# Optimization experiments

Measured on AMD Instinct MI355X. Metric: run time of the kernel, lower is better.

Reference implementation:

```python
import jax, jax.numpy as jnp
import numpy as np

N_NODE = 100000
H = 128          # hidden_size
N_INTEREST = 4
B = 4096         # batch
T = 50           # session length


def setup_inputs() -> dict:
    key = jax.random.key(0)
    ks = jax.random.split(key, 8)
    stdv = 1.0 / np.sqrt(H)
    u = lambda k, s: jax.random.uniform(k, s, jnp.float32, -stdv, stdv)
    return {
        "inputs": jax.random.randint(ks[0], (B, T), 0, N_NODE),
        "embedding": u(ks[1], (N_NODE, H)),            # nn.Embedding weight
        "w_interest": u(ks[2], (N_INTEREST, H)),       # Linear(H -> n_interest, bias=False)
        "w_ih": u(ks[3], (N_INTEREST, 3 * H, H)),      # per-interest GNN params
        "w_hh": u(ks[4], (N_INTEREST, 3 * H, H)),
        "b_ih": u(ks[5], (N_INTEREST, 3 * H)),
        "b_hh": u(ks[6], (N_INTEREST, 3 * H)),
        "h0": jax.random.normal(ks[7], (N_INTEREST, B, H), jnp.float32),  # torch.randn init state
    }


def _gru_interest(w_ih, w_hh, b_ih, b_hh, h0, g_t, x_t):
    """Custom gated recurrence for one interest. x_t: [T,B,H], g_t: [T,B]."""
    def step(h, inp):
        x, gv = inp
        gi = x @ w_ih.T + b_ih          # [B, 3H]
        gh = h @ w_hh.T + b_hh          # [B, 3H]
        i_r, i_i, i_n = jnp.split(gi, 3, axis=1)
        h_r, h_i, h_n = jnp.split(gh, 3, axis=1)
        resetgate = jax.nn.sigmoid(i_r + h_r)
        inputgate = jax.nn.sigmoid(i_i + h_i)
        newgate = jnp.tanh(i_n + resetgate * h_n)
        g = gv[:, None]                  # [B, 1]
        concentrgate = jnp.where(g > 0.01, 1.0, 0.0) * g * inputgate
        hy = (1.0 - concentrgate) * h + concentrgate * newgate
        return hy, None
    h_last, _ = jax.lax.scan(step, h0, (x_t, g_t))
    return h_last                        # [B, H]


def reference(inputs, embedding, w_interest, w_ih, w_hh, b_ih, b_hh, h0):
    hidden = embedding[inputs]                                   # [B, T, H]
    # item_weight_for_interest: softmax over interests with temperature 0.1
    g = jax.nn.softmax((hidden @ w_interest.T) / 0.1, axis=2)    # [B, T, I]
    x_t = jnp.transpose(hidden, (1, 0, 2))                       # [T, B, H]
    g_t = jnp.transpose(g, (2, 1, 0))                            # [I, T, B]
    out = jax.vmap(_gru_interest, in_axes=(0, 0, 0, 0, 0, 0, None))(
        w_ih, w_hh, b_ih, b_hh, h0, g_t, x_t)                    # [I, B, H]
    return jnp.transpose(out, (1, 0, 2))                         # [B, I, H]
```

## Files before the change

### kernel.cpp

```cpp
#include <hip/hip_runtime.h>
#include <hip/hip_bf16.h>

#define NB 4096
#define NT 50
#define NH 128
#define NINT 4
#define ROWS 64

typedef float f32x4 __attribute__((ext_vector_type(4)));
typedef __bf16 bf16x8 __attribute__((ext_vector_type(8)));
typedef short short8 __attribute__((ext_vector_type(8)));
typedef short short4s __attribute__((ext_vector_type(4)));

#define L2E 1.4426950408889634f

__device__ __forceinline__ float frcp(float x) { return __builtin_amdgcn_rcpf(x); }

__device__ __forceinline__ float exp2neg(float x) {
  float r;
  asm("v_exp_f32 %0, -%1" : "=v"(r) : "v"(x));
  return r;
}

__device__ __forceinline__ unsigned short bfbits(float f) {
  __bf16 b = (__bf16)f;
  return __builtin_bit_cast(unsigned short, b);
}

__global__ __launch_bounds__(512, 2)
void gru_fused(const int* __restrict__ inputs, const float* __restrict__ emb,
               const float* __restrict__ w_int, const float* __restrict__ w_ih,
               const float* __restrict__ w_hh, const float* __restrict__ b_ih,
               const float* __restrict__ b_hh, const float* __restrict__ h0,
               float* __restrict__ out) {
  __shared__ unsigned short xs[2][ROWS * NH];
  __shared__ unsigned short hs[2][ROWS * NH];
  __shared__ float gbuf[2][ROWS];
  __shared__ float wintl[NINT][NH + 16];
  __shared__ int idxs[NT * ROWS];

  const int tid = threadIdx.x;
  const int bx = blockIdx.x;
  const int I = bx >> 6;
  const int R0 = (bx & 63) * ROWS;
  const int w = tid >> 6;
  const int lane = tid & 63;
  const int l15 = lane & 15;
  const int l4 = lane >> 4;
  const int oc0 = w * 16 + l4 * 4;

  const int sr = tid >> 3;
  const int sp = tid & 7;

  for (int e = tid; e < NT * ROWS; e += 512) {
    int t = e >> 6, r = e & (ROWS - 1);
    idxs[e] = inputs[(size_t)(R0 + r) * NT + t];
  }
  {
    int i = tid >> 7, f = tid & 127;
    wintl[i][f + ((f >> 5) << 2)] = w_int[tid];
  }
  __syncthreads();

  auto gate_from = [&](int buf, float4 a, float4 b, float4 c, float4 e) {
    const int wbase = sp * 16 + (sp >> 1) * 4;
    float d[NINT];
    #pragma unroll
    for (int i = 0; i < NINT; ++i) {
      const float4* wq = (const float4*)&wintl[i][wbase];
      float4 w0 = wq[0], w1 = wq[1], w2 = wq[2], w3 = wq[3];
      d[i] = a.x * w0.x + a.y * w0.y + a.z * w0.z + a.w * w0.w +
             b.x * w1.x + b.y * w1.y + b.z * w1.z + b.w * w1.w +
             c.x * w2.x + c.y * w2.y + c.z * w2.z + c.w * w2.w +
             e.x * w3.x + e.y * w3.y + e.z * w3.z + e.w * w3.w;
    }
    #pragma unroll
    for (int off = 1; off < 8; off <<= 1) {
      #pragma unroll
      for (int i = 0; i < NINT; ++i) d[i] += __shfl_xor(d[i], off, 64);
    }
    if (sp == 0) {
      float sa = d[0] * 10.f, sb = d[1] * 10.f, sc = d[2] * 10.f, sd = d[3] * 10.f;
      float mx = fmaxf(fmaxf(sa, sb), fmaxf(sc, sd));
      float ea = __expf(sa - mx), eb = __expf(sb - mx), ec = __expf(sc - mx),
            ed = __expf(sd - mx);
      float sel = (I == 0) ? ea : (I == 1) ? eb : (I == 2) ? ec : ed;
      float gv = sel * frcp(ea + eb + ec + ed);
      gbuf[buf][sr] = (gv > 0.01f) ? gv : 0.0f;
    }
  };

  bf16x8 wih[3][4], whh[3][4];
  f32x4 bR, bI, bNI, bNH;
  {
    const float gs[3] = {L2E, L2E, 2.0f * L2E};
    #pragma unroll
    for (int g = 0; g < 3; ++g) {
      int oc = g * NH + w * 16 + l15;
      #pragma unroll
      for (int kk = 0; kk < 4; ++kk) {
        int k0 = kk * 32 + l4 * 8;
        const float* pi = w_ih + ((size_t)(I * 384 + oc) * NH + k0);
        const float* ph = w_hh + ((size_t)(I * 384 + oc) * NH + k0);
        bf16x8 si, sh;
        #pragma unroll
        for (int e = 0; e < 8; ++e) {
          si[e] = (__bf16)(pi[e] * gs[g]);
          sh[e] = (__bf16)(ph[e] * gs[g]);
        }
        wih[g][kk] = si;
        whh[g][kk] = sh;
      }
    }
    #pragma unroll
    for (int j = 0; j < 4; ++j) {
      bR[j] = (b_ih[I * 384 + oc0 + j] + b_hh[I * 384 + oc0 + j]) * L2E;
      bI[j] = (b_ih[I * 384 + NH + oc0 + j] + b_hh[I * 384 + NH + oc0 + j]) * L2E;
      bNI[j] = b_ih[I * 384 + 2 * NH + oc0 + j] * (2.0f * L2E);
      bNH[j] = b_hh[I * 384 + 2 * NH + oc0 + j] * (2.0f * L2E);
    }
  }

  float hm[4][4];
  #pragma unroll
  for (int m = 0; m < 4; ++m) {
    int row = m * 16 + l15;
    short4s p;
    #pragma unroll
    for (int j = 0; j < 4; ++j) {
      float v = h0[((size_t)I * NB + R0 + row) * NH + oc0 + j];
      hm[m][j] = v;
      p[j] = (short)bfbits(v);
    }
    *(short4s*)&hs[0][(row * NH + oc0) ^ ((row & 7) << 3)] = p;
  }

  {
    const float4* src = (const float4*)(emb + (size_t)idxs[sr] * NH + sp * 16);
    float4 v0 = src[0], v1 = src[1], v2 = src[2], v3 = src[3];
    short8 s0, s1;
    s0[0] = bfbits(v0.x); s0[1] = bfbits(v0.y); s0[2] = bfbits(v0.z); s0[3] = bfbits(v0.w);
    s0[4] = bfbits(v1.x); s0[5] = bfbits(v1.y); s0[6] = bfbits(v1.z); s0[7] = bfbits(v1.w);
    s1[0] = bfbits(v2.x); s1[1] = bfbits(v2.y); s1[2] = bfbits(v2.z); s1[3] = bfbits(v2.w);
    s1[4] = bfbits(v3.x); s1[5] = bfbits(v3.y); s1[6] = bfbits(v3.z); s1[7] = bfbits(v3.w);
    int base = sr * NH + sp * 16;
    int sw = (sr & 7) << 3;
    *(short8*)&xs[0][base ^ sw] = s0;
    *(short8*)&xs[0][(base + 8) ^ sw] = s1;
    gate_from(0, v0, v1, v2, v3);
  }
  __syncthreads();

  for (int t = 0; t < NT; ++t) {
    const int cur = t & 1, nxt = cur ^ 1;
    const bool pf = (t + 1 < NT);

    float4 v0, v1, v2, v3;
    if (pf) {
      const float4* src =
          (const float4*)(emb + (size_t)idxs[(t + 1) * ROWS + sr] * NH + sp * 16);
      v0 = src[0]; v1 = src[1]; v2 = src[2]; v3 = src[3];
    }

    const unsigned short* hsc = hs[cur];
    const unsigned short* xsc = xs[cur];
    unsigned short* hsn = hs[nxt];

    #pragma unroll
    for (int m = 0; m < 4; ++m) {
      f32x4 aR = bR, aI = bI, aNI = bNI, aNH = bNH;

      int brow = m * 16 + l15;
      int blin = brow * NH + l4 * 8;
      int sw2 = (brow & 7) << 3;
      __builtin_amdgcn_s_setprio(1);
      #pragma unroll
      for (int kk = 0; kk < 4; ++kk) {
        int e = (blin + kk * 32) ^ sw2;
        bf16x8 bh = __builtin_bit_cast(bf16x8, *(const short8*)&hsc[e]);
        bf16x8 bx = __builtin_bit_cast(bf16x8, *(const short8*)&xsc[e]);
        aR = __builtin_amdgcn_mfma_f32_16x16x32_bf16(wih[0][kk], bx, aR, 0, 0, 0);
        aR = __builtin_amdgcn_mfma_f32_16x16x32_bf16(whh[0][kk], bh, aR, 0, 0, 0);
        aI = __builtin_amdgcn_mfma_f32_16x16x32_bf16(wih[1][kk], bx, aI, 0, 0, 0);
        aI = __builtin_amdgcn_mfma_f32_16x16x32_bf16(whh[1][kk], bh, aI, 0, 0, 0);
        aNI = __builtin_amdgcn_mfma_f32_16x16x32_bf16(wih[2][kk], bx, aNI, 0, 0, 0);
        aNH = __builtin_amdgcn_mfma_f32_16x16x32_bf16(whh[2][kk], bh, aNH, 0, 0, 0);
      }
      __builtin_amdgcn_s_setprio(0);

      const float gv = gbuf[cur][brow];
      short4s p;
      #pragma unroll
      for (int j = 0; j < 4; ++j) {
        float rg = frcp(1.0f + exp2neg(aR[j]));
        float ig = frcp(1.0f + exp2neg(aI[j]));
        float an = fmaf(rg, aNH[j], aNI[j]);
        float ng = fmaf(2.0f, frcp(1.0f + exp2neg(an)), -1.0f);
        float c = gv * ig;
        float hy = fmaf(c, ng - hm[m][j], hm[m][j]);
        hm[m][j] = hy;
        p[j] = (short)bfbits(hy);
      }
      *(short4s*)&hsn[(brow * NH + oc0) ^ sw2] = p;
    }

    if (pf) {
      short8 s0, s1;
      s0[0] = bfbits(v0.x); s0[1] = bfbits(v0.y); s0[2] = bfbits(v0.z); s0[3] = bfbits(v0.w);
      s0[4] = bfbits(v1.x); s0[5] = bfbits(v1.y); s0[6] = bfbits(v1.z); s0[7] = bfbits(v1.w);
      s1[0] = bfbits(v2.x); s1[1] = bfbits(v2.y); s1[2] = bfbits(v2.z); s1[3] = bfbits(v2.w);
      s1[4] = bfbits(v3.x); s1[5] = bfbits(v3.y); s1[6] = bfbits(v3.z); s1[7] = bfbits(v3.w);
      int base = sr * NH + sp * 16;
      int sw = (sr & 7) << 3;
      *(short8*)&xs[nxt][base ^ sw] = s0;
      *(short8*)&xs[nxt][(base + 8) ^ sw] = s1;
      gate_from(nxt, v0, v1, v2, v3);
    }
    __syncthreads();
  }

  #pragma unroll
  for (int m = 0; m < 4; ++m) {
    int row = m * 16 + l15;
    f32x4 o;
    #pragma unroll
    for (int j = 0; j < 4; ++j) o[j] = hm[m][j];
    *(f32x4*)&out[(size_t)(R0 + row) * (NINT * NH) + I * NH + oc0] = o;
  }
}

extern "C" void kernel_launch(void* const* d_in, const int* in_sizes, int n_in,
                              void* d_out, int out_size, void* d_ws, size_t ws_size,
                              hipStream_t stream) {
  const int* inputs = (const int*)d_in[0];
  const float* emb = (const float*)d_in[1];
  const float* w_int = (const float*)d_in[2];
  const float* w_ih = (const float*)d_in[3];
  const float* w_hh = (const float*)d_in[4];
  const float* b_ih = (const float*)d_in[5];
  const float* b_hh = (const float*)d_in[6];
  const float* h0 = (const float*)d_in[7];
  float* out = (float*)d_out;

  dim3 grid(NINT * (NB / ROWS));
  dim3 block(512);
  gru_fused<<<grid, block, 0, stream>>>(inputs, emb, w_int, w_ih, w_hh, b_ih,
                                        b_hh, h0, out);
}
```

Measured before the change: 192.6 us.

## Compute interest softmax gate with MFMA inside the recurrence loop

Replaces the per-step scalar dot-product, shuffle reduction and shared gbuf for the interest softmax gate with an extra bf16 MFMA over the already-staged x tile, using w_interest preloaded into registers (scaled by temperature and log2e). The softmax is then evaluated from the accumulator and broadcast via a lane shuffle. This removes scalar FMA/shuffle work and LDS traffic from the prefetch phase, at the cost of extra redundant MFMAs per wave and bf16 precision on the temperature-sharpened logits.

```diff
diff --git a/kernel.cpp b/kernel.cpp
--- a/kernel.cpp
+++ b/kernel.cpp
@@ -35,8 +35,6 @@
                float* __restrict__ out) {
   __shared__ unsigned short xs[2][ROWS * NH];
   __shared__ unsigned short hs[2][ROWS * NH];
-  __shared__ float gbuf[2][ROWS];
-  __shared__ float wintl[NINT][NH + 16];
   __shared__ int idxs[NT * ROWS];
 
   const int tid = threadIdx.x;
@@ -56,39 +54,7 @@
     int t = e >> 6, r = e & (ROWS - 1);
     idxs[e] = inputs[(size_t)(R0 + r) * NT + t];
   }
-  {
-    int i = tid >> 7, f = tid & 127;
-    wintl[i][f + ((f >> 5) << 2)] = w_int[tid];
-  }
   __syncthreads();
-
-  auto gate_from = [&](int buf, float4 a, float4 b, float4 c, float4 e) {
-    const int wbase = sp * 16 + (sp >> 1) * 4;
-    float d[NINT];
-    #pragma unroll
-    for (int i = 0; i < NINT; ++i) {
-      const float4* wq = (const float4*)&wintl[i][wbase];
-      float4 w0 = wq[0], w1 = wq[1], w2 = wq[2], w3 = wq[3];
-      d[i] = a.x * w0.x + a.y * w0.y + a.z * w0.z + a.w * w0.w +
-             b.x * w1.x + b.y * w1.y + b.z * w1.z + b.w * w1.w +
-             c.x * w2.x + c.y * w2.y + c.z * w2.z + c.w * w2.w +
-             e.x * w3.x + e.y * w3.y + e.z * w3.z + e.w * w3.w;
-    }
-    #pragma unroll
-    for (int off = 1; off < 8; off <<= 1) {
-      #pragma unroll
-      for (int i = 0; i < NINT; ++i) d[i] += __shfl_xor(d[i], off, 64);
-    }
-    if (sp == 0) {
-      float sa = d[0] * 10.f, sb = d[1] * 10.f, sc = d[2] * 10.f, sd = d[3] * 10.f;
-      float mx = fmaxf(fmaxf(sa, sb), fmaxf(sc, sd));
-      float ea = __expf(sa - mx), eb = __expf(sb - mx), ec = __expf(sc - mx),
-            ed = __expf(sd - mx);
-      float sel = (I == 0) ? ea : (I == 1) ? eb : (I == 2) ? ec : ed;
-      float gv = sel * frcp(ea + eb + ec + ed);
-      gbuf[buf][sr] = (gv > 0.01f) ? gv : 0.0f;
-    }
-  };
 
   bf16x8 wih[3][4], whh[3][4];
   f32x4 bR, bI, bNI, bNH;
@@ -121,6 +87,20 @@
     }
   }
 
+  bf16x8 wg[4];
+  #pragma unroll
+  for (int kk = 0; kk < 4; ++kk) {
+    bf16x8 f;
+    #pragma unroll
+    for (int e = 0; e < 8; ++e) {
+      float v = (l15 < NINT)
+                    ? w_int[l15 * NH + kk * 32 + l4 * 8 + e] * (10.0f * L2E)
+                    : 0.0f;
+      f[e] = (__bf16)v;
+    }
+    wg[kk] = f;
+  }
+
   float hm[4][4];
   #pragma unroll
   for (int m = 0; m < 4; ++m) {
@@ -147,7 +127,6 @@
     int sw = (sr & 7) << 3;
     *(short8*)&xs[0][base ^ sw] = s0;
     *(short8*)&xs[0][(base + 8) ^ sw] = s1;
-    gate_from(0, v0, v1, v2, v3);
   }
   __syncthreads();
 
@@ -169,6 +148,7 @@
     #pragma unroll
     for (int m = 0; m < 4; ++m) {
       f32x4 aR = bR, aI = bI, aNI = bNI, aNH = bNH;
+      f32x4 aG = f32x4{0.0f, 0.0f, 0.0f, 0.0f};
 
       int brow = m * 16 + l15;
       int blin = brow * NH + l4 * 8;
@@ -179,6 +159,7 @@
         int e = (blin + kk * 32) ^ sw2;
         bf16x8 bh = __builtin_bit_cast(bf16x8, *(const short8*)&hsc[e]);
         bf16x8 bx = __builtin_bit_cast(bf16x8, *(const short8*)&xsc[e]);
+        aG = __builtin_amdgcn_mfma_f32_16x16x32_bf16(wg[kk], bx, aG, 0, 0, 0);
         aR = __builtin_amdgcn_mfma_f32_16x16x32_bf16(wih[0][kk], bx, aR, 0, 0, 0);
         aR = __builtin_amdgcn_mfma_f32_16x16x32_bf16(whh[0][kk], bh, aR, 0, 0, 0);
         aI = __builtin_amdgcn_mfma_f32_16x16x32_bf16(wih[1][kk], bx, aI, 0, 0, 0);
@@ -188,7 +169,15 @@
       }
       __builtin_amdgcn_s_setprio(0);
 
-      const float gv = gbuf[cur][brow];
+      float s0 = aG[0], s1 = aG[1], s2 = aG[2], s3 = aG[3];
+      float mx = fmaxf(fmaxf(s0, s1), fmaxf(s2, s3));
+      float e0 = exp2neg(mx - s0), e1 = exp2neg(mx - s1);
+      float e2 = exp2neg(mx - s2), e3 = exp2neg(mx - s3);
+      float sel = (I == 0) ? e0 : (I == 1) ? e1 : (I == 2) ? e2 : e3;
+      float gvl = sel * frcp(e0 + e1 + e2 + e3);
+      gvl = (gvl > 0.01f) ? gvl : 0.0f;
+      const float gv = __shfl(gvl, l15, 64);
+
       short4s p;
       #pragma unroll
       for (int j = 0; j < 4; ++j) {
@@ -214,7 +203,6 @@
       int sw = (sr & 7) << 3;
       *(short8*)&xs[nxt][base ^ sw] = s0;
       *(short8*)&xs[nxt][(base + 8) ^ sw] = s1;
-      gate_from(nxt, v0, v1, v2, v3);
     }
     __syncthreads();
   }
```

After: 193.0 us. Within noise of the previous version (+0.2%).
